# Kernel tuning notes

Measured on AMD Instinct MI355X. Metric: run time of the kernel, lower is better.

The kernel has to match this reference:

```python
import jax, jax.numpy as jnp
import numpy as np
from jax import lax

# sign binarization to {-1,+1} with straight-through estimator (standard BNN binarizePM1)
@jax.custom_vjp
def binarize(x):
    return jnp.where(x >= 0, 1.0, -1.0).astype(x.dtype)

def _bin_fwd(x):
    return binarize(x), None

def _bin_bwd(_, g):
    return (g,)  # straight-through

binarize.defvjp(_bin_fwd, _bin_bwd)

def conv2d(x, w, b):
    # NCHW, OIHW, 3x3, stride 1, pad 1
    y = lax.conv_general_dilated(x, w, window_strides=(1, 1), padding=((1, 1), (1, 1)),
                                 dimension_numbers=('NCHW', 'OIHW', 'NCHW'))
    return y + b[None, :, None, None]

def maxpool2(x):
    return lax.reduce_window(x, -jnp.inf, lax.max, (1, 1, 2, 2), (1, 1, 2, 2), 'VALID')

def bn(x, gamma, beta, mean, var, eps=1e-5):
    # inference-mode batchnorm; broadcasts over channel axis 1 (4D) or feature axis 1 (2D)
    if x.ndim == 4:
        shp = (1, -1, 1, 1)
    else:
        shp = (1, -1)
    inv = gamma * lax.rsqrt(var + eps)
    return x * inv.reshape(shp) + (beta - mean * inv).reshape(shp)

def setup_inputs() -> dict:
    key = jax.random.key(0)
    ks = jax.random.split(key, 16)
    B = 4096
    d = {}
    d['x'] = jax.random.normal(ks[0], (B, 1, 28, 28), jnp.float32)
    d['conv1_w'] = jax.random.normal(ks[1], (64, 1, 3, 3), jnp.float32) * 0.1
    d['conv1_b'] = jax.random.normal(ks[2], (64,), jnp.float32) * 0.01
    d['conv2_w'] = jax.random.normal(ks[3], (64, 64, 3, 3), jnp.float32) * 0.05
    d['conv2_b'] = jax.random.normal(ks[4], (64,), jnp.float32) * 0.01
    d['fc1_w'] = jax.random.normal(ks[5], (2048, 7 * 7 * 64), jnp.float32) * 0.02
    d['fc1_b'] = jax.random.normal(ks[6], (2048,), jnp.float32) * 0.01
    d['fc2_w'] = jax.random.normal(ks[7], (10, 2048), jnp.float32) * 0.02
    d['fc2_b'] = jax.random.normal(ks[8], (10,), jnp.float32) * 0.01
    for i, (name, c) in enumerate([('bn1', 64), ('bn2', 64), ('bn3', 2048)]):
        d[name + '_gamma'] = jnp.ones((c,), jnp.float32)
        d[name + '_beta'] = jnp.zeros((c,), jnp.float32)
        d[name + '_mean'] = jax.random.normal(ks[9 + i], (c,), jnp.float32) * 0.1
        d[name + '_var'] = jax.random.uniform(ks[12 + i], (c,), jnp.float32, 0.5, 1.5)
    d['scale'] = jnp.array([1e-5], jnp.float32)
    return d

def reference(x, conv1_w, conv1_b, conv2_w, conv2_b, fc1_w, fc1_b, fc2_w, fc2_b,
              bn1_gamma, bn1_beta, bn1_mean, bn1_var,
              bn2_gamma, bn2_beta, bn2_mean, bn2_var,
              bn3_gamma, bn3_beta, bn3_mean, bn3_var, scale):
    h = conv2d(x, binarize(conv1_w), conv1_b)          # [B,64,28,28]
    h = maxpool2(h)                                    # [B,64,14,14]
    h = bn(h, bn1_gamma, bn1_beta, bn1_mean, bn1_var)
    h = jnp.clip(h, -1.0, 1.0)                         # hardtanh
    h = binarize(h)                                    # qact1
    h = conv2d(h, binarize(conv2_w), conv2_b)          # [B,64,14,14]
    h = maxpool2(h)                                    # [B,64,7,7]
    h = bn(h, bn2_gamma, bn2_beta, bn2_mean, bn2_var)
    h = jnp.clip(h, -1.0, 1.0)
    h = binarize(h)
    h = h.reshape(h.shape[0], -1)                      # [B,3136]
    h = h @ binarize(fc1_w).T + fc1_b                  # [B,2048]
    h = bn(h, bn3_gamma, bn3_beta, bn3_mean, bn3_var)
    h = jnp.clip(h, -1.0, 1.0)
    h = binarize(h)
    h = h @ binarize(fc2_w).T + fc2_b                  # [B,10]
    return h * scale
```

## Files before the change

### kernel.cpp

```cpp
#include <hip/hip_runtime.h>
#include <stdint.h>

typedef unsigned long long ULL;


__global__ void prep_sgn1(const float* __restrict__ w1, float* __restrict__ sgn1) {
    int t = blockIdx.x * 256 + threadIdx.x;
    if (t < 576) sgn1[t] = (w1[t] >= 0.f) ? 1.f : -1.f;
}

__global__ void prep_pack_small(const float* __restrict__ w2, const float* __restrict__ fc2w,
                                ULL* __restrict__ wb2, ULL* __restrict__ wbf2) {
    int wave = threadIdx.x >> 6, lane = threadIdx.x & 63;
    int W = blockIdx.x * 4 + wave;
    if (W < 576) {
        int co = W / 9, tap = W - co * 9;
        ULL wd = __ballot(w2[(co * 64 + lane) * 9 + tap] >= 0.f);
        if (lane == 0) wb2[W] = wd;
    } else if (W < 576 + 320) {
        int idx = W - 576;
        int n = idx >> 5, k = idx & 31;
        ULL wd = __ballot(fc2w[n * 2048 + k * 64 + lane] >= 0.f);
        if (lane == 0) wbf2[idx] = wd;
    }
}

__global__ __launch_bounds__(256) void prep_pack_fc1(const float* __restrict__ fc1w,
                                                     ULL* __restrict__ wbT) {
    __shared__ float rows[4 * 3136];
    int t = threadIdx.x;
    const float* src = fc1w + (size_t)blockIdx.x * 4 * 3136;
    for (int i = t; i < 4 * 3136; i += 256) rows[i] = src[i];
    __syncthreads();
    int wave = t >> 6, lane = t & 63;
    int n = blockIdx.x * 4 + wave;
    const float* r = rows + wave * 3136 + lane * 49;
    for (int p = 0; p < 49; ++p) {
        ULL wd = __ballot(r[p] >= 0.f);
        if (lane == 0) wbT[p * 2048 + n] = wd;
    }
}

__global__ __launch_bounds__(448) void k1_conv1(const float* __restrict__ x,
        const float* __restrict__ sgn1, const float* __restrict__ b1,
        const float* __restrict__ g, const float* __restrict__ be,
        const float* __restrict__ mu, const float* __restrict__ va,
        ULL* __restrict__ qact1) {
    __shared__ float limg[30 * 30];
    int b = blockIdx.x, t = threadIdx.x;
    int wave = t >> 6, lane = t & 63;
    for (int i = t; i < 900; i += 448) limg[i] = 0.f;
    __syncthreads();
    const float* xb = x + (size_t)b * 784;
    for (int i = t; i < 784; i += 448) {
        int y = i / 28, xx = i - y * 28;
        limg[(xx + 1) * 30 + (y + 1)] = xb[i];
    }
    float w[9];
    #pragma unroll
    for (int k = 0; k < 9; ++k) w[k] = sgn1[lane * 9 + k];
    double iv = (double)g[lane] / sqrt((double)va[lane] + 1e-5);
    double cd = (double)be[lane] - (double)mu[lane] * iv;
    double bd = (double)b1[lane];
    __syncthreads();

    #pragma unroll
    for (int rr = 0; rr < 2; ++rr) {
        int py = wave + rr * 7;
        float win[4][4];
        #pragma unroll
        for (int c = 0; c < 2; ++c) {
            const float2* cp = (const float2*)&limg[c * 30 + 2 * py];
            float2 lo = cp[0], hi = cp[1];
            win[0][c] = lo.x; win[1][c] = lo.y; win[2][c] = hi.x; win[3][c] = hi.y;
        }
        for (int px = 0; px < 14; ++px) {
            #pragma unroll
            for (int c = 0; c < 2; ++c) {
                const float2* cp = (const float2*)&limg[(2 * px + 2 + c) * 30 + 2 * py];
                float2 lo = cp[0], hi = cp[1];
                win[0][2 + c] = lo.x; win[1][2 + c] = lo.y; win[2][2 + c] = hi.x; win[3][2 + c] = hi.y;
            }
            float a00 = 0.f, a01 = 0.f, a10 = 0.f, a11 = 0.f;
            #pragma unroll
            for (int ky = 0; ky < 3; ++ky) {
                #pragma unroll
                for (int kx = 0; kx < 3; ++kx) {
                    float sv = w[ky * 3 + kx];
                    a00 = fmaf(win[ky][kx],         sv, a00);
                    a01 = fmaf(win[ky][kx + 1],     sv, a01);
                    a10 = fmaf(win[ky + 1][kx],     sv, a10);
                    a11 = fmaf(win[ky + 1][kx + 1], sv, a11);
                }
            }
            float m = fmaxf(fmaxf(a00, a01), fmaxf(a10, a11));
            double v  = (double)m + bd;
            double tt = v * iv + cd;
            ULL word = __ballot(tt >= 0.0);
            if (lane == 0) qact1[(size_t)b * 196 + py * 14 + px] = word;
            #pragma unroll
            for (int r = 0; r < 4; ++r) {
                win[r][0] = win[r][2];
                win[r][1] = win[r][3];
            }
        }
    }
}

__global__ __launch_bounds__(448) void k2_conv2(const ULL* __restrict__ qact1,
        const ULL* __restrict__ wb2, const float* __restrict__ b2,
        const float* __restrict__ g, const float* __restrict__ be,
        const float* __restrict__ mu, const float* __restrict__ va,
        ULL* __restrict__ qact2) {
    __shared__ ULL ap[16][16];
    int b = blockIdx.x, t = threadIdx.x;
    int pr = t >> 6, lane = t & 63;
    if (t < 256) ap[t >> 4][t & 15] = 0ULL;
    __syncthreads();
    if (t < 196) ap[1 + t / 14][1 + t % 14] = qact1[(size_t)b * 196 + t];

    ULL wk[9];
    #pragma unroll
    for (int k = 0; k < 9; ++k) wk[k] = wb2[lane * 9 + k];
    int pw[9];
    #pragma unroll
    for (int k = 0; k < 9; ++k) pw[k] = 64 - 2 * (int)__popcll(wk[k]);
    double iv   = (double)g[lane] / sqrt((double)va[lane] + 1e-5);
    double cc   = (double)be[lane] - (double)mu[lane] * iv;
    double bias = (double)b2[lane];

    int corr[2][3];
    #pragma unroll
    for (int j = 0; j < 2; ++j) {
        bool tpad = (pr == 0 && j == 0);
        bool bpad = (pr == 6 && j == 1);
        #pragma unroll
        for (int cls = 0; cls < 3; ++cls) {
            int cacc = 0;
            #pragma unroll
            for (int r = 0; r < 3; ++r) {
                #pragma unroll
                for (int k = 0; k < 3; ++k) {
                    bool pad = (r == 0 && tpad) || (r == 2 && bpad) ||
                               (k == 0 && cls == 0) || (k == 2 && cls == 2);
                    if (pad) cacc += pw[r * 3 + k];
                }
            }
            corr[j][cls] = cacc;
        }
    }
    __syncthreads();

    ULL win[4][4];
    #pragma unroll
    for (int r = 0; r < 4; ++r) {
        win[r][0] = ap[2 * pr + r][0];
        win[r][1] = ap[2 * pr + r][1];
    }
    for (int px = 0; px < 7; ++px) {
        #pragma unroll
        for (int r = 0; r < 4; ++r) {
            win[r][2] = ap[2 * pr + r][2 * px + 2];
            win[r][3] = ap[2 * pr + r][2 * px + 3];
        }
        int s00 = 0, s01 = 0, s10 = 0, s11 = 0;
        #pragma unroll
        for (int r = 0; r < 3; ++r) {
            #pragma unroll
            for (int k = 0; k < 3; ++k) {
                ULL w = wk[r * 3 + k];
                s00 += (int)__popcll(win[r][k]         ^ w);
                s01 += (int)__popcll(win[r][k + 1]     ^ w);
                s10 += (int)__popcll(win[r + 1][k]     ^ w);
                s11 += (int)__popcll(win[r + 1][k + 1] ^ w);
            }
        }
        int clsL = (px == 0) ? 0 : 1, clsR = (px == 6) ? 2 : 1;
        int d00 = 576 - 2 * s00 - corr[0][clsL];
        int d01 = 576 - 2 * s01 - corr[0][clsR];
        int d10 = 576 - 2 * s10 - corr[1][clsL];
        int d11 = 576 - 2 * s11 - corr[1][clsR];
        int m = max(max(d00, d01), max(d10, d11));
        double tt = ((double)m + bias) * iv + cc;
        ULL word = __ballot(tt >= 0.0);
        if (lane == 0) qact2[(size_t)b * 49 + pr * 7 + px] = word;
        #pragma unroll
        for (int r = 0; r < 4; ++r) {
            win[r][0] = win[r][2];
            win[r][1] = win[r][3];
        }
    }
}

__global__ __launch_bounds__(256) void k3_fc1(const ULL* __restrict__ qact2,
        const ULL* __restrict__ wbT, const float* __restrict__ fb,
        const float* __restrict__ g, const float* __restrict__ be,
        const float* __restrict__ mu, const float* __restrict__ va,
        ULL* __restrict__ hbits) {
    __shared__ ULL xs[784];
    int t = threadIdx.x, wave = t >> 6, lane = t & 63;
    int b0 = blockIdx.x * 16;
    int gidx = blockIdx.y * 4 + wave;
    int n = gidx * 64 + lane;
    for (int i = t; i < 784; i += 256) xs[i] = qact2[(size_t)b0 * 49 + i];
    double iv   = (double)g[n] / sqrt((double)va[n] + 1e-5);
    double cc   = (double)be[n] - (double)mu[n] * iv;
    double bias = (double)fb[n];
    __syncthreads();
    int acc[16];
    #pragma unroll
    for (int i = 0; i < 16; ++i) acc[i] = 0;
    for (int p = 0; p < 49; ++p) {
        ULL w = wbT[p * 2048 + n];
        #pragma unroll
        for (int i = 0; i < 16; ++i)
            acc[i] += (int)__popcll(xs[i * 49 + p] ^ w);
    }
    #pragma unroll
    for (int i = 0; i < 16; ++i) {
        int dot = 3136 - 2 * acc[i];
        double tt = ((double)dot + bias) * iv + cc;
        ULL word = __ballot(tt >= 0.0);
        if (lane == 0) hbits[(size_t)(b0 + i) * 32 + gidx] = word;
    }
}

__global__ __launch_bounds__(256) void k4_fc2(const ULL* __restrict__ hbits,
        const ULL* __restrict__ wbf2, const float* __restrict__ b2,
        const float* __restrict__ scale, float* __restrict__ out, int total) {
    int gid = blockIdx.x * 256 + threadIdx.x;
    if (gid >= total) return;
    int b = gid / 10, n = gid - b * 10;
    const ULL* h = hbits + (size_t)b * 32;
    const ULL* w = wbf2 + n * 32;
    int acc = 0;
    #pragma unroll
    for (int k = 0; k < 32; ++k) acc += (int)__popcll(h[k] ^ w[k]);
    int dot = 2048 - 2 * acc;
    double v = ((double)dot + (double)b2[n]) * (double)scale[0];
    out[gid] = (float)v;
}

extern "C" void kernel_launch(void* const* d_in, const int* in_sizes, int n_in,
                              void* d_out, int out_size, void* d_ws, size_t ws_size,
                              hipStream_t stream) {
    const float* x      = (const float*)d_in[0];
    const float* w1     = (const float*)d_in[1];
    const float* b1     = (const float*)d_in[2];
    const float* w2     = (const float*)d_in[3];
    const float* b2     = (const float*)d_in[4];
    const float* fc1w   = (const float*)d_in[5];
    const float* fc1b   = (const float*)d_in[6];
    const float* fc2w   = (const float*)d_in[7];
    const float* fc2b   = (const float*)d_in[8];
    const float* g1 = (const float*)d_in[9],  *be1 = (const float*)d_in[10],
               *mu1 = (const float*)d_in[11], *va1 = (const float*)d_in[12];
    const float* g2 = (const float*)d_in[13], *be2 = (const float*)d_in[14],
               *mu2 = (const float*)d_in[15], *va2 = (const float*)d_in[16];
    const float* g3 = (const float*)d_in[17], *be3 = (const float*)d_in[18],
               *mu3 = (const float*)d_in[19], *va3 = (const float*)d_in[20];
    const float* scale = (const float*)d_in[21];
    float* out = (float*)d_out;

    int B = in_sizes[0] / 784;

    char* ws = (char*)d_ws;
    ULL* qact1 = (ULL*)(ws);
    ULL* qact2 = (ULL*)(ws + (size_t)B * 196 * 8);
    ULL* hbits = (ULL*)(ws + (size_t)B * 245 * 8);
    char* wsw  = ws + (size_t)B * 277 * 8;
    ULL* wb2   = (ULL*)(wsw);
    ULL* wbT   = (ULL*)(wsw + 576 * 8);
    ULL* wbf2  = (ULL*)(wsw + 576 * 8 + 49 * 2048 * 8);
    float* sgn1 = (float*)(wsw + 576 * 8 + 49 * 2048 * 8 + 320 * 8);

    prep_sgn1<<<3, 256, 0, stream>>>(w1, sgn1);
    prep_pack_small<<<224, 256, 0, stream>>>(w2, fc2w, wb2, wbf2);
    prep_pack_fc1<<<512, 256, 0, stream>>>(fc1w, wbT);

    k1_conv1<<<B, 448, 0, stream>>>(x, sgn1, b1, g1, be1, mu1, va1, qact1);
    k2_conv2<<<B, 448, 0, stream>>>(qact1, wb2, b2, g2, be2, mu2, va2, qact2);
    k3_fc1<<<dim3(B / 16, 8), 256, 0, stream>>>(qact2, wbT, fc1b, g3, be3, mu3, va3, hbits);
    int total = B * 10;
    k4_fc2<<<(total + 255) / 256, 256, 0, stream>>>(hbits, wbf2, fc2b, scale, out, total);
}
```

Baseline: 312.9 us.

## Merge prep kernels, read conv windows from LDS, precompute integer BN thresholds

```diff
diff --git a/kernel.cpp b/kernel.cpp
--- a/kernel.cpp
+++ b/kernel.cpp
@@ -3,25 +3,23 @@
 
 typedef unsigned long long ULL;
 
-
-__global__ void prep_sgn1(const float* __restrict__ w1, float* __restrict__ sgn1) {
-    int t = blockIdx.x * 256 + threadIdx.x;
-    if (t < 576) sgn1[t] = (w1[t] >= 0.f) ? 1.f : -1.f;
-}
-
-__global__ void prep_pack_small(const float* __restrict__ w2, const float* __restrict__ fc2w,
-                                ULL* __restrict__ wb2, ULL* __restrict__ wbf2) {
+__global__ __launch_bounds__(256) void prep_small(const float* __restrict__ w1,
+        const float* __restrict__ w2, const float* __restrict__ fc2w,
+        float* __restrict__ sgn1, ULL* __restrict__ wb2, ULL* __restrict__ wbf2) {
     int wave = threadIdx.x >> 6, lane = threadIdx.x & 63;
     int W = blockIdx.x * 4 + wave;
     if (W < 576) {
         int co = W / 9, tap = W - co * 9;
         ULL wd = __ballot(w2[(co * 64 + lane) * 9 + tap] >= 0.f);
         if (lane == 0) wb2[W] = wd;
-    } else if (W < 576 + 320) {
+    } else if (W < 896) {
         int idx = W - 576;
         int n = idx >> 5, k = idx & 31;
         ULL wd = __ballot(fc2w[n * 2048 + k * 64 + lane] >= 0.f);
         if (lane == 0) wbf2[idx] = wd;
+    } else if (W < 905) {
+        int i = (W - 896) * 64 + lane;
+        if (i < 576) sgn1[i] = (w1[i] >= 0.f) ? 1.f : -1.f;
     }
 }
 
@@ -41,7 +39,7 @@
     }
 }
 
-__global__ __launch_bounds__(448) void k1_conv1(const float* __restrict__ x,
+__global__ __launch_bounds__(448, 4) void k1_conv1(const float* __restrict__ x,
         const float* __restrict__ sgn1, const float* __restrict__ b1,
         const float* __restrict__ g, const float* __restrict__ be,
         const float* __restrict__ mu, const float* __restrict__ va,
@@ -67,30 +65,19 @@
     #pragma unroll
     for (int rr = 0; rr < 2; ++rr) {
         int py = wave + rr * 7;
-        float win[4][4];
-        #pragma unroll
-        for (int c = 0; c < 2; ++c) {
-            const float2* cp = (const float2*)&limg[c * 30 + 2 * py];
-            float2 lo = cp[0], hi = cp[1];
-            win[0][c] = lo.x; win[1][c] = lo.y; win[2][c] = hi.x; win[3][c] = hi.y;
-        }
+        const float* base = &limg[2 * py];
+        #pragma unroll
         for (int px = 0; px < 14; ++px) {
-            #pragma unroll
-            for (int c = 0; c < 2; ++c) {
-                const float2* cp = (const float2*)&limg[(2 * px + 2 + c) * 30 + 2 * py];
-                float2 lo = cp[0], hi = cp[1];
-                win[0][2 + c] = lo.x; win[1][2 + c] = lo.y; win[2][2 + c] = hi.x; win[3][2 + c] = hi.y;
-            }
             float a00 = 0.f, a01 = 0.f, a10 = 0.f, a11 = 0.f;
             #pragma unroll
             for (int ky = 0; ky < 3; ++ky) {
                 #pragma unroll
                 for (int kx = 0; kx < 3; ++kx) {
                     float sv = w[ky * 3 + kx];
-                    a00 = fmaf(win[ky][kx],         sv, a00);
-                    a01 = fmaf(win[ky][kx + 1],     sv, a01);
-                    a10 = fmaf(win[ky + 1][kx],     sv, a10);
-                    a11 = fmaf(win[ky + 1][kx + 1], sv, a11);
+                    a00 = fmaf(base[(2 * px + kx)     * 30 + ky],     sv, a00);
+                    a01 = fmaf(base[(2 * px + kx + 1) * 30 + ky],     sv, a01);
+                    a10 = fmaf(base[(2 * px + kx)     * 30 + ky + 1], sv, a10);
+                    a11 = fmaf(base[(2 * px + kx + 1) * 30 + ky + 1], sv, a11);
                 }
             }
             float m = fmaxf(fmaxf(a00, a01), fmaxf(a10, a11));
@@ -98,16 +85,11 @@
             double tt = v * iv + cd;
             ULL word = __ballot(tt >= 0.0);
             if (lane == 0) qact1[(size_t)b * 196 + py * 14 + px] = word;
-            #pragma unroll
-            for (int r = 0; r < 4; ++r) {
-                win[r][0] = win[r][2];
-                win[r][1] = win[r][3];
-            }
         }
     }
 }
 
-__global__ __launch_bounds__(448) void k2_conv2(const ULL* __restrict__ qact1,
+__global__ __launch_bounds__(448, 4) void k2_conv2(const ULL* __restrict__ qact1,
         const ULL* __restrict__ wb2, const float* __restrict__ b2,
         const float* __restrict__ g, const float* __restrict__ be,
         const float* __restrict__ mu, const float* __restrict__ va,
@@ -115,7 +97,7 @@
     __shared__ ULL ap[16][16];
     int b = blockIdx.x, t = threadIdx.x;
     int pr = t >> 6, lane = t & 63;
-    if (t < 256) ap[t >> 4][t & 15] = 0ULL;
+    if (t < 256) ((ULL*)ap)[t] = 0ULL;
     __syncthreads();
     if (t < 196) ap[1 + t / 14][1 + t % 14] = qact1[(size_t)b * 196 + t];
 
@@ -125,9 +107,27 @@
     int pw[9];
     #pragma unroll
     for (int k = 0; k < 9; ++k) pw[k] = 64 - 2 * (int)__popcll(wk[k]);
+
     double iv   = (double)g[lane] / sqrt((double)va[lane] + 1e-5);
     double cc   = (double)be[lane] - (double)mu[lane] * iv;
     double bias = (double)b2[lane];
+    int am, thr;
+    if (iv > 0.0) {
+        double t0 = -cc / iv - bias;
+        int c = (t0 < -590.0) ? -590 : (t0 > 590.0 ? 590 : (int)floor(t0) - 2);
+        if (c < -590) c = -590;
+        while (c <= 590 && !(((double)c + bias) * iv + cc >= 0.0)) ++c;
+        am = 1; thr = c;
+    } else if (iv < 0.0) {
+        double t0 = -cc / iv - bias;
+        int c = (t0 > 590.0) ? 590 : (t0 < -590.0 ? -590 : (int)ceil(t0) + 2);
+        if (c > 590) c = 590;
+        while (c >= -590 && !(((double)c + bias) * iv + cc >= 0.0)) --c;
+        am = -1; thr = c;
+    } else {
+        am = 1; thr = (cc >= 0.0) ? -1000000 : 1000000;
+    }
+    int athr = am * thr;
 
     int corr[2][3];
     #pragma unroll
@@ -151,44 +151,29 @@
     }
     __syncthreads();
 
-    ULL win[4][4];
-    #pragma unroll
-    for (int r = 0; r < 4; ++r) {
-        win[r][0] = ap[2 * pr + r][0];
-        win[r][1] = ap[2 * pr + r][1];
-    }
+    const ULL* aprow = &ap[2 * pr][0];
+    #pragma unroll
     for (int px = 0; px < 7; ++px) {
-        #pragma unroll
-        for (int r = 0; r < 4; ++r) {
-            win[r][2] = ap[2 * pr + r][2 * px + 2];
-            win[r][3] = ap[2 * pr + r][2 * px + 3];
-        }
         int s00 = 0, s01 = 0, s10 = 0, s11 = 0;
         #pragma unroll
         for (int r = 0; r < 3; ++r) {
             #pragma unroll
             for (int k = 0; k < 3; ++k) {
                 ULL w = wk[r * 3 + k];
-                s00 += (int)__popcll(win[r][k]         ^ w);
-                s01 += (int)__popcll(win[r][k + 1]     ^ w);
-                s10 += (int)__popcll(win[r + 1][k]     ^ w);
-                s11 += (int)__popcll(win[r + 1][k + 1] ^ w);
+                s00 += (int)__popcll(aprow[ r      * 16 + 2 * px + k    ] ^ w);
+                s01 += (int)__popcll(aprow[ r      * 16 + 2 * px + k + 1] ^ w);
+                s10 += (int)__popcll(aprow[(r + 1) * 16 + 2 * px + k    ] ^ w);
+                s11 += (int)__popcll(aprow[(r + 1) * 16 + 2 * px + k + 1] ^ w);
             }
         }
-        int clsL = (px == 0) ? 0 : 1, clsR = (px == 6) ? 2 : 1;
+        const int clsL = (px == 0) ? 0 : 1, clsR = (px == 6) ? 2 : 1;
         int d00 = 576 - 2 * s00 - corr[0][clsL];
         int d01 = 576 - 2 * s01 - corr[0][clsR];
         int d10 = 576 - 2 * s10 - corr[1][clsL];
         int d11 = 576 - 2 * s11 - corr[1][clsR];
         int m = max(max(d00, d01), max(d10, d11));
-        double tt = ((double)m + bias) * iv + cc;
-        ULL word = __ballot(tt >= 0.0);
+        ULL word = __ballot(am * m >= athr);
         if (lane == 0) qact2[(size_t)b * 49 + pr * 7 + px] = word;
-        #pragma unroll
-        for (int r = 0; r < 4; ++r) {
-            win[r][0] = win[r][2];
-            win[r][1] = win[r][3];
-        }
     }
 }
 
@@ -274,8 +259,7 @@
     ULL* wbf2  = (ULL*)(wsw + 576 * 8 + 49 * 2048 * 8);
     float* sgn1 = (float*)(wsw + 576 * 8 + 49 * 2048 * 8 + 320 * 8);
 
-    prep_sgn1<<<3, 256, 0, stream>>>(w1, sgn1);
-    prep_pack_small<<<224, 256, 0, stream>>>(w2, fc2w, wb2, wbf2);
+    prep_small<<<227, 256, 0, stream>>>(w1, w2, fc2w, sgn1, wb2, wbf2);
     prep_pack_fc1<<<512, 256, 0, stream>>>(fc1w, wbT);
 
     k1_conv1<<<B, 448, 0, stream>>>(x, sgn1, b1, g1, be1, mu1, va1, qact1);
```

Result: no change. 314.2 us (+0.4%).
